# Optimization experiments

Measured on AMD Instinct MI355X. Metric: run time of the kernel, lower is better.

The kernel has to match this reference:

```python
import jax, jax.numpy as jnp
import numpy as np

K = 9          # top-k neighbors
GROUPS = 4     # GroupNorm groups
EPS_GN = 1e-5  # torch GroupNorm default eps


def group_norm(x, gamma, beta):
    # x: [B, C, H, W]; normalize over (C/GROUPS, H, W) per group
    B, C, H, W = x.shape
    xg = x.reshape(B, GROUPS, -1)
    mu = xg.mean(axis=-1, keepdims=True)
    var = xg.var(axis=-1, keepdims=True)
    xn = ((xg - mu) / jnp.sqrt(var + EPS_GN)).reshape(B, C, H, W)
    return xn * gamma[None, :, None, None] + beta[None, :, None, None]


def setup_inputs() -> dict:
    key = jax.random.key(0)
    ks = jax.random.split(key, 6)
    B, C, H, W = 32, 128, 45, 45
    std = 1.0 / np.sqrt(C)
    x = jax.random.normal(ks[0], (B, C, H, W), dtype=jnp.float32)
    w1 = jax.random.uniform(ks[1], (C, C), jnp.float32, -std, std)
    b1 = jax.random.uniform(ks[2], (C,), jnp.float32, -std, std)
    w2 = jax.random.uniform(ks[3], (C, C), jnp.float32, -std, std)
    b2 = jax.random.uniform(ks[4], (C,), jnp.float32, -std, std)
    gamma1 = jnp.ones((C,), jnp.float32)
    beta1 = jnp.zeros((C,), jnp.float32)
    gamma2 = jnp.ones((C,), jnp.float32)
    beta2 = jnp.zeros((C,), jnp.float32)
    return {"x": x, "w1": w1, "b1": b1, "w2": w2, "b2": b2,
            "gamma1": gamma1, "beta1": beta1, "gamma2": gamma2, "beta2": beta2}


def reference(x, w1, b1, w2, b2, gamma1, beta1, gamma2, beta2):
    B, C, H, W = x.shape
    N = H * W
    # build_knn: flatten, L2-normalize, cosine sim, top-k
    xf = x.reshape(B, C, N).transpose(0, 2, 1)                  # [B, N, C]
    nrm = jnp.linalg.norm(xf, axis=-1, keepdims=True)
    xn = xf / jnp.maximum(nrm, 1e-12)                           # F.normalize
    sim = jnp.einsum('bnc,bmc->bnm', xn, xn)                    # [B, N, N]
    val, idx = jax.lax.top_k(sim, K)                            # [B, N, K]
    # normalized edge weights (shared by both GCN layers)
    v = val / (val.sum(axis=-1, keepdims=True) + 1e-6)          # [B, N, K]

    def gcn_apply(feat, w, b):
        xt = feat @ w                                           # [B, N, C]
        neigh = jax.vmap(lambda t, i: t[i])(xt, idx)            # [B, N, K, C]
        return jnp.einsum('bnkc,bnk->bnc', neigh, v) + b

    out = gcn_apply(xn, w1, b1)
    out = jax.nn.silu(group_norm(out.transpose(0, 2, 1).reshape(B, C, H, W), gamma1, beta1))
    of = out.reshape(B, C, N).transpose(0, 2, 1)
    out = gcn_apply(of, w2, b2)
    out = jax.nn.silu(group_norm(out.transpose(0, 2, 1).reshape(B, C, H, W), gamma2, beta2))
    return out
```

## Files before the change

### kernel.cpp

```cpp
#include <hip/hip_runtime.h>
#include <hip/hip_bf16.h>

#define BN 32
#define CC 128
#define NN 2025
#define KK 9
#define NGROUP 4
#define CPG 32
#define GN_EPS 1e-5f
#define ROWS_TOTAL (BN * NN)

typedef _Float16 f16;
typedef __attribute__((ext_vector_type(8))) _Float16 f16x8;
typedef __attribute__((ext_vector_type(4))) _Float16 f16x4;
typedef __attribute__((ext_vector_type(4))) float f32x4;

#define S28 3.725290298461914e-09f
#define S40 9.094947017729282e-13f
#define S26 1.4901161193847656e-08f
#define S38 3.637978807091713e-12f
#define RH  6.103515625e-05f
#define RL  1.4901161193847656e-08f

#define T0F 0.17f
#define CAP 100

__global__ __launch_bounds__(256) void k_normalize(const float* __restrict__ x,
                                                   f16* __restrict__ xh, f16* __restrict__ xl) {
    __shared__ float tile[128][65];
    const int b  = blockIdx.y;
    const int n0 = blockIdx.x * 64;
    const int t  = threadIdx.x;
    const int w  = t >> 6;
    const int lane = t & 63;
    const int gn_ld = min(n0 + lane, NN - 1);

    for (int it = 0; it < 32; ++it) {
        int c = it * 4 + w;
        tile[c][lane] = x[((size_t)(b * CC + c)) * NN + gn_ld];
    }
    __syncthreads();

    for (int i = 0; i < 16; ++i) {
        int n  = w * 16 + i;
        int gn = n0 + n;
        if (gn < NN) {
            float v0 = tile[lane][n];
            float v1 = tile[lane + 64][n];
            float ss = v0 * v0 + v1 * v1;
#pragma unroll
            for (int off = 32; off > 0; off >>= 1) ss += __shfl_xor(ss, off);
            float s = 1.0f / fmaxf(sqrtf(ss), 1e-12f);
            v0 *= s; v1 *= s;
            float w0 = v0 * 16384.0f, w1 = v1 * 16384.0f;
            f16 h0 = (f16)w0, h1 = (f16)w1;
            f16 l0 = (f16)((w0 - (float)h0) * 4096.0f);
            f16 l1 = (f16)((w1 - (float)h1) * 4096.0f);
            size_t base = (size_t)(b * NN + gn) * CC;
            xh[base + lane] = h0;  xh[base + lane + 64] = h1;
            xl[base + lane] = l0;  xl[base + lane + 64] = l1;
        }
    }
}

__device__ __forceinline__ void ins9(float cand, int m, float* v, int* ix,
                                     float& mv, int& mi, int& mp) {
    bool take = (cand > mv) || ((cand == mv) && (m < mi));
    if (take) {
#pragma unroll
        for (int k = 0; k < 9; ++k) if (k == mp) { v[k] = cand; ix[k] = m; }
        float nv = v[0]; int ni = ix[0]; int np = 0;
#pragma unroll
        for (int k = 1; k < 9; ++k) {
            if (v[k] < nv || (v[k] == nv && ix[k] > ni)) { nv = v[k]; ni = ix[k]; np = k; }
        }
        mv = nv; mi = ni; mp = np;
    }
}

__global__ __launch_bounds__(256) void k_sim_topk(const f16* __restrict__ xh, const f16* __restrict__ xl,
                                                  float* __restrict__ vout, unsigned short* __restrict__ iout) {
    __shared__ f16x8          stg[2][32][16];
    __shared__ float          sv[32][CAP + 1];
    __shared__ unsigned short si[32][CAP + 2];
    __shared__ int   cnt[32];
    __shared__ int   nbad;
    __shared__ int   badrows[32];

    const int id   = blockIdx.x;
    const int b    = (id & 7) + 8 * (id >> 9);
    const int r0   = ((id >> 3) & 63) * 32;
    const int t    = threadIdx.x;
    const int w    = t >> 6;
    const int lane = t & 63;
    const int jr   = lane & 15;
    const int q    = lane >> 4;
    const int tw   = w & 1;
    const int mh   = w >> 1;

    if (t < 32) cnt[t] = 0;
    if (t == 0) nbad = 0;

    f16x8 bh[4], bl[4];
    {
        int rr = b * NN + min(r0 + tw * 16 + jr, NN - 1);
        const f16* pH = xh + (size_t)rr * CC;
        const f16* pL = xl + (size_t)rr * CC;
#pragma unroll
        for (int s = 0; s < 4; ++s) {
            bh[s] = *(const f16x8*)(pH + s * 32 + q * 8);
            bl[s] = *(const f16x8*)(pL + s * 32 + q * 8);
        }
    }

    const int fi_ = t & 15;
    const int ri_ = t >> 4;
    const int fx  = fi_ ^ (ri_ & 7);
    const int rbuf = tw * 16 + jr;

    f16x8 h0r, h1r, l0r, l1r;
    {
        size_t g0 = (size_t)(b * NN + min(ri_, NN - 1)) * CC + fi_ * 8;
        size_t g1 = (size_t)(b * NN + min(ri_ + 16, NN - 1)) * CC + fi_ * 8;
        h0r = *(const f16x8*)(xh + g0);  h1r = *(const f16x8*)(xh + g1);
        l0r = *(const f16x8*)(xl + g0);  l1r = *(const f16x8*)(xl + g1);
    }

    for (int chunk = 0; chunk < 64; ++chunk) {
        __syncthreads();
        stg[0][ri_][fx]      = h0r;
        stg[0][ri_ + 16][fx] = h1r;
        stg[1][ri_][fx]      = l0r;
        stg[1][ri_ + 16][fx] = l1r;
        __syncthreads();
        if (chunk < 63) {
            size_t g0 = (size_t)(b * NN + min((chunk + 1) * 32 + ri_, NN - 1)) * CC + fi_ * 8;
            size_t g1 = (size_t)(b * NN + min((chunk + 1) * 32 + ri_ + 16, NN - 1)) * CC + fi_ * 8;
            h0r = *(const f16x8*)(xh + g0);  h1r = *(const f16x8*)(xh + g1);
            l0r = *(const f16x8*)(xl + g0);  l1r = *(const f16x8*)(xl + g1);
        }
        __builtin_amdgcn_sched_barrier(0);

        const int mb   = chunk * 32 + mh * 16;
        const int arow = mh * 16 + jr;
        const int axr  = arow & 7;
        f32x4 hh = {0.f, 0.f, 0.f, 0.f}, ll = {0.f, 0.f, 0.f, 0.f};
#pragma unroll
        for (int s = 0; s < 4; ++s) {
            f16x8 ah = stg[0][arow][(s * 4 + q) ^ axr];
            f16x8 al = stg[1][arow][(s * 4 + q) ^ axr];
            hh = __builtin_amdgcn_mfma_f32_16x16x32_f16(ah, bh[s], hh, 0, 0, 0);
            ll = __builtin_amdgcn_mfma_f32_16x16x32_f16(ah, bl[s], ll, 0, 0, 0);
            ll = __builtin_amdgcn_mfma_f32_16x16x32_f16(al, bh[s], ll, 0, 0, 0);
        }
#pragma unroll
        for (int reg = 0; reg < 4; ++reg) {
            int m = mb + q * 4 + reg;
            float c0 = hh[reg] * S28 + ll[reg] * S40;
            if (m < NN && c0 > T0F) {
                int pos = atomicAdd(&cnt[rbuf], 1);
                if (pos < CAP) { sv[rbuf][pos] = c0; si[rbuf][pos] = (unsigned short)m; }
            }
        }
    }
    __syncthreads();

    if (t < 32) {
        int r = r0 + t;
        if (r < NN) {
            int c = cnt[t];
            if (c >= 9 && c <= CAP) {
                float fv[9]; int fi[9];
#pragma unroll
                for (int k = 0; k < 9; ++k) { fv[k] = -3.0e38f; fi[k] = 0x7fffffff; }
                float mv = -3.0e38f; int mi = 0x7fffffff; int mp = 0;
                for (int j = 0; j < c; ++j) ins9(sv[t][j], (int)si[t][j], fv, fi, mv, mi, mp);
                float s = 1e-6f;
#pragma unroll
                for (int k = 0; k < 9; ++k) s += fv[k];
                float inv = 1.0f / s;
                int base = (b * NN + r) * KK;
#pragma unroll
                for (int k = 0; k < 9; ++k) { vout[base + k] = fv[k] * inv; iout[base + k] = (unsigned short)fi[k]; }
            } else {
                int slot = atomicAdd(&nbad, 1);
                badrows[slot] = r;
            }
        }
    }
    __syncthreads();

    if (w == 0) {
        int nb = nbad;
        for (int ib = 0; ib < nb; ++ib) {
            int r = badrows[ib];
            const f16* rH = xh + ((size_t)b * NN + r) * CC;
            const f16* rL = xl + ((size_t)b * NN + r) * CC;
            float fv[9]; int fi[9];
#pragma unroll
            for (int k = 0; k < 9; ++k) { fv[k] = -3.0e38f; fi[k] = 0x7fffffff; }
            float mv = -3.0e38f; int mi = 0x7fffffff; int mp = 0;
            for (int m = lane; m < NN; m += 64) {
                const f16* mH = xh + ((size_t)b * NN + m) * CC;
                const f16* mL = xl + ((size_t)b * NN + m) * CC;
                float a1 = 0.f, a2 = 0.f;
                for (int c2 = 0; c2 < CC; ++c2) {
                    float hr = (float)rH[c2], hm = (float)mH[c2];
                    float lr = (float)rL[c2], lm = (float)mL[c2];
                    a1 += hr * hm;
                    a2 += hr * lm + lr * hm;
                }
                ins9(a1 * S28 + a2 * S40, m, fv, fi, mv, mi, mp);
            }
#pragma unroll
            for (int off = 1; off < 64; off <<= 1) {
                float pv[9]; int pi[9];
#pragma unroll
                for (int k = 0; k < 9; ++k) { pv[k] = __shfl_xor(fv[k], off); pi[k] = __shfl_xor(fi[k], off); }
#pragma unroll
                for (int k = 0; k < 9; ++k) ins9(pv[k], pi[k], fv, fi, mv, mi, mp);
            }
            if (lane == 0) {
                float s = 1e-6f;
#pragma unroll
                for (int k = 0; k < 9; ++k) s += fv[k];
                float inv = 1.0f / s;
                int base = (b * NN + r) * KK;
#pragma unroll
                for (int k = 0; k < 9; ++k) { vout[base + k] = fv[k] * inv; iout[base + k] = (unsigned short)fi[k]; }
            }
        }
    }
}

__global__ __launch_bounds__(256) void k_wsplit(const float* __restrict__ w1, const float* __restrict__ w2,
                                                f16* __restrict__ wth1, f16* __restrict__ wtl1,
                                                f16* __restrict__ wth2, f16* __restrict__ wtl2) {
    const float* w = blockIdx.x ? w2 : w1;
    f16* th = blockIdx.x ? wth2 : wth1;
    f16* tl = blockIdx.x ? wtl2 : wtl1;
    for (int e = threadIdx.x; e < CC * CC; e += 256) {
        int c = e >> 7, j = e & 127;
        float ws_ = w[e] * 16384.0f;
        f16 h = (f16)ws_;
        f16 l = (f16)((ws_ - (float)h) * 4096.0f);
        th[j * CC + c] = h;
        tl[j * CC + c] = l;
    }
}

__global__ __launch_bounds__(256) void k_gemm_mf(const f16* __restrict__ ah, const f16* __restrict__ al,
                                                 const f16* __restrict__ wth, const f16* __restrict__ wtl,
                                                 float sH, float sL, float* __restrict__ out) {
    const int t    = threadIdx.x;
    const int w    = t >> 6;
    const int lane = t & 63;
    const int jr   = lane & 15;
    const int q    = lane >> 4;
    const int row0 = blockIdx.x * 32;

    f16x8 wbh[2][4], wbl[2][4];
#pragma unroll
    for (int ct = 0; ct < 2; ++ct) {
        int j = w * 32 + ct * 16 + jr;
        const f16* pH = wth + (size_t)j * CC;
        const f16* pL = wtl + (size_t)j * CC;
#pragma unroll
        for (int s = 0; s < 4; ++s) {
            wbh[ct][s] = *(const f16x8*)(pH + s * 32 + q * 8);
            wbl[ct][s] = *(const f16x8*)(pL + s * 32 + q * 8);
        }
    }

#pragma unroll
    for (int rt = 0; rt < 2; ++rt) {
        int arow = row0 + rt * 16 + jr;
        const f16* pA  = ah + (size_t)arow * CC;
        const f16* pAl = al + (size_t)arow * CC;
        f16x8 af[4], alf[4];
#pragma unroll
        for (int s = 0; s < 4; ++s) {
            af[s]  = *(const f16x8*)(pA  + s * 32 + q * 8);
            alf[s] = *(const f16x8*)(pAl + s * 32 + q * 8);
        }
        f32x4 hh0 = {0.f,0.f,0.f,0.f}, ll0 = {0.f,0.f,0.f,0.f};
        f32x4 hh1 = {0.f,0.f,0.f,0.f}, ll1 = {0.f,0.f,0.f,0.f};
#pragma unroll
        for (int s = 0; s < 4; ++s) {
            hh0 = __builtin_amdgcn_mfma_f32_16x16x32_f16(af[s],  wbh[0][s], hh0, 0, 0, 0);
            ll0 = __builtin_amdgcn_mfma_f32_16x16x32_f16(af[s],  wbl[0][s], ll0, 0, 0, 0);
            ll0 = __builtin_amdgcn_mfma_f32_16x16x32_f16(alf[s], wbh[0][s], ll0, 0, 0, 0);
            hh1 = __builtin_amdgcn_mfma_f32_16x16x32_f16(af[s],  wbh[1][s], hh1, 0, 0, 0);
            ll1 = __builtin_amdgcn_mfma_f32_16x16x32_f16(af[s],  wbl[1][s], ll1, 0, 0, 0);
            ll1 = __builtin_amdgcn_mfma_f32_16x16x32_f16(alf[s], wbh[1][s], ll1, 0, 0, 0);
        }
#pragma unroll
        for (int reg = 0; reg < 4; ++reg) {
            int orow = row0 + rt * 16 + q * 4 + reg;
            size_t ob = (size_t)orow * CC + w * 32 + jr;
            out[ob]      = hh0[reg] * sH + ll0[reg] * sL;
            out[ob + 16] = hh1[reg] * sH + ll1[reg] * sL;
        }
    }
}

__global__ __launch_bounds__(256) void k_gather(const float* __restrict__ xt,
                                                const float* __restrict__ v,
                                                const unsigned short* __restrict__ idx,
                                                const float* __restrict__ bias,
                                                float* __restrict__ out) {
    int t = threadIdx.x;
    int g = blockIdx.x * 2 + (t >> 7);
    int c = t & 127;
    if (g >= ROWS_TOTAL) return;
    int b = g / NN;
    int nb = b * NN;
    float acc = bias[c];
    int base = g * KK;
#pragma unroll
    for (int k = 0; k < KK; ++k) {
        int   ii = (int)idx[base + k];
        float vv = v[base + k];
        acc += vv * xt[(size_t)(nb + ii) * CC + c];
    }
    out[(size_t)g * CC + c] = acc;
}

__global__ __launch_bounds__(256) void k_gnstats(const float* __restrict__ xin,
                                                 float* __restrict__ stats) {
    int bg = blockIdx.x; int b = bg >> 2; int gg = bg & 3;
    size_t base = (size_t)b * (NN * CC) + gg * CPG;
    float s1 = 0.f, s2 = 0.f;
    for (int i = threadIdx.x; i < NN * CPG; i += 256) {
        float x = xin[base + (size_t)(i >> 5) * CC + (i & 31)];
        s1 += x; s2 += x * x;
    }
#pragma unroll
    for (int off = 32; off > 0; off >>= 1) { s1 += __shfl_xor(s1, off); s2 += __shfl_xor(s2, off); }
    __shared__ float r1[4], r2[4];
    int w = threadIdx.x >> 6;
    if ((threadIdx.x & 63) == 0) { r1[w] = s1; r2[w] = s2; }
    __syncthreads();
    if (threadIdx.x == 0) {
        float a = r1[0] + r1[1] + r1[2] + r1[3];
        float qq = r2[0] + r2[1] + r2[2] + r2[3];
        const float inv = 1.0f / (float)(NN * CPG);
        float mean = a * inv;
        float var = qq * inv - mean * mean;
        stats[bg * 2]     = mean;
        stats[bg * 2 + 1] = rsqrtf(fmaxf(var, 0.f) + GN_EPS);
    }
}

__global__ __launch_bounds__(256) void k_gnsilu_split(const float* __restrict__ xin,
                                                      const float* __restrict__ stats,
                                                      const float* __restrict__ gamma,
                                                      const float* __restrict__ beta,
                                                      f16* __restrict__ vh, f16* __restrict__ vl) {
    size_t e4 = ((size_t)blockIdx.x * 256 + threadIdx.x) * 4;
    int c0 = (int)(e4 & 127);
    int b  = (int)(e4 / (NN * CC));
    int gg = c0 >> 5;
    float mean = stats[(b * 4 + gg) * 2];
    float rstd = stats[(b * 4 + gg) * 2 + 1];
    float4 x = *(const float4*)&xin[e4];
    float g0 = gamma[c0], g1 = gamma[c0 + 1], g2 = gamma[c0 + 2], g3 = gamma[c0 + 3];
    float p0 = beta[c0],  p1 = beta[c0 + 1],  p2 = beta[c0 + 2],  p3 = beta[c0 + 3];
    float y0 = (x.x - mean) * rstd * g0 + p0;
    float y1 = (x.y - mean) * rstd * g1 + p1;
    float y2 = (x.z - mean) * rstd * g2 + p2;
    float y3 = (x.w - mean) * rstd * g3 + p3;
    float r0 = y0 / (1.0f + expf(-y0));
    float r1 = y1 / (1.0f + expf(-y1));
    float r2 = y2 / (1.0f + expf(-y2));
    float r3 = y3 / (1.0f + expf(-y3));
    f16x4 hv, lv;
    float s0 = r0 * 4096.0f; hv[0] = (f16)s0; lv[0] = (f16)((s0 - (float)hv[0]) * 4096.0f);
    float s1 = r1 * 4096.0f; hv[1] = (f16)s1; lv[1] = (f16)((s1 - (float)hv[1]) * 4096.0f);
    float s2 = r2 * 4096.0f; hv[2] = (f16)s2; lv[2] = (f16)((s2 - (float)hv[2]) * 4096.0f);
    float s3 = r3 * 4096.0f; hv[3] = (f16)s3; lv[3] = (f16)((s3 - (float)hv[3]) * 4096.0f);
    *(f16x4*)&vh[e4] = hv;
    *(f16x4*)&vl[e4] = lv;
}

__global__ __launch_bounds__(256) void k_gnsilu_out(const float* __restrict__ xin,
                                                    const float* __restrict__ stats,
                                                    const float* __restrict__ gamma,
                                                    const float* __restrict__ beta,
                                                    float* __restrict__ out) {
    __shared__ float tile[32 * 65];
    int b = blockIdx.z, ct = blockIdx.y, nt = blockIdx.x;
    int c0 = ct * 32, n0 = nt * 64;
    int t = threadIdx.x;
    int cj = t & 31, ni0 = t >> 5;
    int gg = c0 >> 5;
    float mean = stats[(b * 4 + gg) * 2];
    float rstd = stats[(b * 4 + gg) * 2 + 1];
    float gm = gamma[c0 + cj];
    float bt = beta[c0 + cj];
#pragma unroll
    for (int i = 0; i < 8; ++i) {
        int n = n0 + ni0 + i * 8;
        if (n < NN) {
            float x = xin[((size_t)b * NN + n) * CC + c0 + cj];
            float y = (x - mean) * rstd * gm + bt;
            y = y / (1.0f + expf(-y));
            tile[cj * 65 + ni0 + i * 8] = y;
        }
    }
    __syncthreads();
    int nj = t & 63, ci0 = t >> 6;
#pragma unroll
    for (int i = 0; i < 8; ++i) {
        int c = ci0 + i * 4;
        int n = n0 + nj;
        if (n < NN) out[((size_t)b * CC + c0 + c) * NN + n] = tile[c * 65 + nj];
    }
}

extern "C" void kernel_launch(void* const* d_in, const int* in_sizes, int n_in,
                              void* d_out, int out_size, void* d_ws, size_t ws_size,
                              hipStream_t stream) {
    const float* x      = (const float*)d_in[0];
    const float* w1     = (const float*)d_in[1];
    const float* b1     = (const float*)d_in[2];
    const float* w2     = (const float*)d_in[3];
    const float* b2     = (const float*)d_in[4];
    const float* gamma1 = (const float*)d_in[5];
    const float* beta1  = (const float*)d_in[6];
    const float* gamma2 = (const float*)d_in[7];
    const float* beta2  = (const float*)d_in[8];
    float* out = (float*)d_out;

    const size_t BIG = (size_t)ROWS_TOTAL * CC;
    const size_t RK  = (size_t)ROWS_TOTAL * KK;
    float* ws   = (float*)d_ws;
    float* bufB = ws;
    f16*   xh   = (f16*)(ws + BIG);
    f16*   xl   = xh + BIG;
    float* bufA = ws + BIG;
    float* vbuf = ws + 2 * BIG;
    unsigned short* ibuf = (unsigned short*)(ws + 2 * BIG + RK);
    f16*   wth1 = (f16*)(ws + 2 * BIG + RK + RK / 2);
    f16*   wtl1 = wth1 + CC * CC;
    f16*   wth2 = wtl1 + CC * CC;
    f16*   wtl2 = wth2 + CC * CC;
    float* stats = ws + 2 * BIG + RK + RK / 2 + 2 * CC * CC;
    f16*   vh = (f16*)bufB;
    f16*   vl = vh + BIG;

    k_normalize<<<dim3(32, BN), 256, 0, stream>>>(x, xh, xl);
    k_wsplit<<<2, 256, 0, stream>>>(w1, w2, wth1, wtl1, wth2, wtl2);
    k_sim_topk<<<2048, 256, 0, stream>>>(xh, xl, vbuf, ibuf);

    k_gemm_mf<<<ROWS_TOTAL / 32, 256, 0, stream>>>(xh, xl, wth1, wtl1, S28, S40, bufB);
    k_gather<<<ROWS_TOTAL / 2, 256, 0, stream>>>(bufB, vbuf, ibuf, b1, bufA);
    k_gnstats<<<BN * NGROUP, 256, 0, stream>>>(bufA, stats);
    k_gnsilu_split<<<(int)(BIG / 1024), 256, 0, stream>>>(bufA, stats, gamma1, beta1, vh, vl);

    k_gemm_mf<<<ROWS_TOTAL / 32, 256, 0, stream>>>(vh, vl, wth2, wtl2, S26, S38, bufA);
    k_gather<<<ROWS_TOTAL / 2, 256, 0, stream>>>(bufA, vbuf, ibuf, b2, bufB);
    k_gnstats<<<BN * NGROUP, 256, 0, stream>>>(bufB, stats);
    k_gnsilu_out<<<dim3((NN + 63) / 64, NGROUP, BN), 256, 0, stream>>>(bufB, stats, gamma2, beta2, out);
}
```

Measured before the change: 671.6 us.

## Fuse GroupNorm+SiLU split into second GEMM and tile GEMM through swizzled LDS

Replaces the GEMM with a version that processes 128 rows per block in 32-row chunks. A-operand tiles are staged through XOR-swizzled shared memory, and the next chunk is prefetched into registers while the current one computes. Weight fragments are loaded once per block instead of once per 32 rows. The layer-1 GroupNorm+SiLU+fp16 split kernel is folded into the second GEMM's staging step, which removes a full write and read of the split activation buffers. The cost is more per-thread work (expf and splitting) inside the GEMM and fewer blocks.

```diff
diff --git a/kernel.cpp b/kernel.cpp
--- a/kernel.cpp
+++ b/kernel.cpp
@@ -12,15 +12,12 @@
 
 typedef _Float16 f16;
 typedef __attribute__((ext_vector_type(8))) _Float16 f16x8;
-typedef __attribute__((ext_vector_type(4))) _Float16 f16x4;
 typedef __attribute__((ext_vector_type(4))) float f32x4;
 
 #define S28 3.725290298461914e-09f
 #define S40 9.094947017729282e-13f
 #define S26 1.4901161193847656e-08f
 #define S38 3.637978807091713e-12f
-#define RH  6.103515625e-05f
-#define RL  1.4901161193847656e-08f
 
 #define T0F 0.17f
 #define CAP 100
@@ -249,15 +246,16 @@
     }
 }
 
-__global__ __launch_bounds__(256) void k_gemm_mf(const f16* __restrict__ ah, const f16* __restrict__ al,
-                                                 const f16* __restrict__ wth, const f16* __restrict__ wtl,
-                                                 float sH, float sL, float* __restrict__ out) {
+__global__ __launch_bounds__(256) void k_gemm_tile(const f16* __restrict__ ah, const f16* __restrict__ al,
+                                                   const f16* __restrict__ wth, const f16* __restrict__ wtl,
+                                                   float sH, float sL, float* __restrict__ out) {
+    __shared__ f16x8 stg[2][32][16];
     const int t    = threadIdx.x;
     const int w    = t >> 6;
     const int lane = t & 63;
     const int jr   = lane & 15;
     const int q    = lane >> 4;
-    const int row0 = blockIdx.x * 32;
+    const int row0 = blockIdx.x * 128;
 
     f16x8 wbh[2][4], wbl[2][4];
 #pragma unroll
@@ -272,34 +270,179 @@
         }
     }
 
-#pragma unroll
-    for (int rt = 0; rt < 2; ++rt) {
-        int arow = row0 + rt * 16 + jr;
-        const f16* pA  = ah + (size_t)arow * CC;
-        const f16* pAl = al + (size_t)arow * CC;
-        f16x8 af[4], alf[4];
+    const int fi_ = t & 15;
+    const int ri_ = t >> 4;
+    const int fx  = fi_ ^ (ri_ & 7);
+
+    f16x8 h0r, h1r, l0r, l1r;
+    {
+        size_t g0 = (size_t)min(row0 + ri_, ROWS_TOTAL - 1) * CC + fi_ * 8;
+        size_t g1 = (size_t)min(row0 + ri_ + 16, ROWS_TOTAL - 1) * CC + fi_ * 8;
+        h0r = *(const f16x8*)(ah + g0);  h1r = *(const f16x8*)(ah + g1);
+        l0r = *(const f16x8*)(al + g0);  l1r = *(const f16x8*)(al + g1);
+    }
+
+    for (int chunk = 0; chunk < 4; ++chunk) {
+        __syncthreads();
+        stg[0][ri_][fx]      = h0r;
+        stg[0][ri_ + 16][fx] = h1r;
+        stg[1][ri_][fx]      = l0r;
+        stg[1][ri_ + 16][fx] = l1r;
+        __syncthreads();
+        if (chunk < 3) {
+            size_t g0 = (size_t)min(row0 + (chunk + 1) * 32 + ri_, ROWS_TOTAL - 1) * CC + fi_ * 8;
+            size_t g1 = (size_t)min(row0 + (chunk + 1) * 32 + ri_ + 16, ROWS_TOTAL - 1) * CC + fi_ * 8;
+            h0r = *(const f16x8*)(ah + g0);  h1r = *(const f16x8*)(ah + g1);
+            l0r = *(const f16x8*)(al + g0);  l1r = *(const f16x8*)(al + g1);
+        }
+        __builtin_amdgcn_sched_barrier(0);
+
+#pragma unroll
+        for (int rt = 0; rt < 2; ++rt) {
+            const int arow = rt * 16 + jr;
+            const int axr  = arow & 7;
+            f16x8 af[4], alf[4];
+#pragma unroll
+            for (int s = 0; s < 4; ++s) {
+                af[s]  = stg[0][arow][(s * 4 + q) ^ axr];
+                alf[s] = stg[1][arow][(s * 4 + q) ^ axr];
+            }
+            f32x4 hh0 = {0.f,0.f,0.f,0.f}, ll0 = {0.f,0.f,0.f,0.f};
+            f32x4 hh1 = {0.f,0.f,0.f,0.f}, ll1 = {0.f,0.f,0.f,0.f};
+#pragma unroll
+            for (int s = 0; s < 4; ++s) {
+                hh0 = __builtin_amdgcn_mfma_f32_16x16x32_f16(af[s],  wbh[0][s], hh0, 0, 0, 0);
+                ll0 = __builtin_amdgcn_mfma_f32_16x16x32_f16(af[s],  wbl[0][s], ll0, 0, 0, 0);
+                ll0 = __builtin_amdgcn_mfma_f32_16x16x32_f16(alf[s], wbh[0][s], ll0, 0, 0, 0);
+                hh1 = __builtin_amdgcn_mfma_f32_16x16x32_f16(af[s],  wbh[1][s], hh1, 0, 0, 0);
+                ll1 = __builtin_amdgcn_mfma_f32_16x16x32_f16(af[s],  wbl[1][s], ll1, 0, 0, 0);
+                ll1 = __builtin_amdgcn_mfma_f32_16x16x32_f16(alf[s], wbh[1][s], ll1, 0, 0, 0);
+            }
+#pragma unroll
+            for (int reg = 0; reg < 4; ++reg) {
+                int orow = row0 + chunk * 32 + rt * 16 + q * 4 + reg;
+                if (orow < ROWS_TOTAL) {
+                    size_t ob = (size_t)orow * CC + w * 32 + jr;
+                    out[ob]      = hh0[reg] * sH + ll0[reg] * sL;
+                    out[ob + 16] = hh1[reg] * sH + ll1[reg] * sL;
+                }
+            }
+        }
+    }
+}
+
+__global__ __launch_bounds__(256) void k_gemm_tile_gn(const float* __restrict__ act,
+                                                      const float* __restrict__ stats,
+                                                      const float* __restrict__ gamma,
+                                                      const float* __restrict__ beta,
+                                                      const f16* __restrict__ wth, const f16* __restrict__ wtl,
+                                                      float sH, float sL, float* __restrict__ out) {
+    __shared__ f16x8 stg[2][32][16];
+    const int t    = threadIdx.x;
+    const int w    = t >> 6;
+    const int lane = t & 63;
+    const int jr   = lane & 15;
+    const int q    = lane >> 4;
+    const int row0 = blockIdx.x * 128;
+
+    f16x8 wbh[2][4], wbl[2][4];
+#pragma unroll
+    for (int ct = 0; ct < 2; ++ct) {
+        int j = w * 32 + ct * 16 + jr;
+        const f16* pH = wth + (size_t)j * CC;
+        const f16* pL = wtl + (size_t)j * CC;
 #pragma unroll
         for (int s = 0; s < 4; ++s) {
-            af[s]  = *(const f16x8*)(pA  + s * 32 + q * 8);
-            alf[s] = *(const f16x8*)(pAl + s * 32 + q * 8);
-        }
-        f32x4 hh0 = {0.f,0.f,0.f,0.f}, ll0 = {0.f,0.f,0.f,0.f};
-        f32x4 hh1 = {0.f,0.f,0.f,0.f}, ll1 = {0.f,0.f,0.f,0.f};
-#pragma unroll
-        for (int s = 0; s < 4; ++s) {
-            hh0 = __builtin_amdgcn_mfma_f32_16x16x32_f16(af[s],  wbh[0][s], hh0, 0, 0, 0);
-            ll0 = __builtin_amdgcn_mfma_f32_16x16x32_f16(af[s],  wbl[0][s], ll0, 0, 0, 0);
-            ll0 = __builtin_amdgcn_mfma_f32_16x16x32_f16(alf[s], wbh[0][s], ll0, 0, 0, 0);
-            hh1 = __builtin_amdgcn_mfma_f32_16x16x32_f16(af[s],  wbh[1][s], hh1, 0, 0, 0);
-            ll1 = __builtin_amdgcn_mfma_f32_16x16x32_f16(af[s],  wbl[1][s], ll1, 0, 0, 0);
-            ll1 = __builtin_amdgcn_mfma_f32_16x16x32_f16(alf[s], wbh[1][s], ll1, 0, 0, 0);
-        }
-#pragma unroll
-        for (int reg = 0; reg < 4; ++reg) {
-            int orow = row0 + rt * 16 + q * 4 + reg;
-            size_t ob = (size_t)orow * CC + w * 32 + jr;
-            out[ob]      = hh0[reg] * sH + ll0[reg] * sL;
-            out[ob + 16] = hh1[reg] * sH + ll1[reg] * sL;
+            wbh[ct][s] = *(const f16x8*)(pH + s * 32 + q * 8);
+            wbl[ct][s] = *(const f16x8*)(pL + s * 32 + q * 8);
+        }
+    }
+
+    const int fi_ = t & 15;
+    const int ri_ = t >> 4;
+    const int fx  = fi_ ^ (ri_ & 7);
+    const int gg  = fi_ >> 2;
+
+    float gma[8], bta[8];
+#pragma unroll
+    for (int e = 0; e < 8; ++e) { gma[e] = gamma[fi_ * 8 + e]; bta[e] = beta[fi_ * 8 + e]; }
+
+    float4 pa0, pa1, pb0, pb1;
+    int ra = min(row0 + ri_, ROWS_TOTAL - 1);
+    int rb = min(row0 + ri_ + 16, ROWS_TOTAL - 1);
+    {
+        const float* p0 = act + (size_t)ra * CC + fi_ * 8;
+        const float* p1 = act + (size_t)rb * CC + fi_ * 8;
+        pa0 = *(const float4*)p0;  pa1 = *(const float4*)(p0 + 4);
+        pb0 = *(const float4*)p1;  pb1 = *(const float4*)(p1 + 4);
+    }
+
+    for (int chunk = 0; chunk < 4; ++chunk) {
+        __syncthreads();
+        {
+            float va[8] = {pa0.x, pa0.y, pa0.z, pa0.w, pa1.x, pa1.y, pa1.z, pa1.w};
+            float vb[8] = {pb0.x, pb0.y, pb0.z, pb0.w, pb1.x, pb1.y, pb1.z, pb1.w};
+            int ba = ra / NN, bb = rb / NN;
+            float ma = stats[(ba * 4 + gg) * 2], rsa = stats[(ba * 4 + gg) * 2 + 1];
+            float mb = stats[(bb * 4 + gg) * 2], rsb = stats[(bb * 4 + gg) * 2 + 1];
+            f16x8 hva, lva, hvb, lvb;
+#pragma unroll
+            for (int e = 0; e < 8; ++e) {
+                float ya = (va[e] - ma) * rsa * gma[e] + bta[e];
+                float ra_ = ya / (1.0f + expf(-ya));
+                float sa = ra_ * 4096.0f;
+                f16 h = (f16)sa; hva[e] = h; lva[e] = (f16)((sa - (float)h) * 4096.0f);
+                float yb = (vb[e] - mb) * rsb * gma[e] + bta[e];
+                float rb_ = yb / (1.0f + expf(-yb));
+                float sb = rb_ * 4096.0f;
+                f16 h2 = (f16)sb; hvb[e] = h2; lvb[e] = (f16)((sb - (float)h2) * 4096.0f);
+            }
+            stg[0][ri_][fx]      = hva;
+            stg[0][ri_ + 16][fx] = hvb;
+            stg[1][ri_][fx]      = lva;
+            stg[1][ri_ + 16][fx] = lvb;
+        }
+        __syncthreads();
+        if (chunk < 3) {
+            ra = min(row0 + (chunk + 1) * 32 + ri_, ROWS_TOTAL - 1);
+            rb = min(row0 + (chunk + 1) * 32 + ri_ + 16, ROWS_TOTAL - 1);
+            const float* p0 = act + (size_t)ra * CC + fi_ * 8;
+            const float* p1 = act + (size_t)rb * CC + fi_ * 8;
+            pa0 = *(const float4*)p0;  pa1 = *(const float4*)(p0 + 4);
+            pb0 = *(const float4*)p1;  pb1 = *(const float4*)(p1 + 4);
+        }
+        __builtin_amdgcn_sched_barrier(0);
+
+#pragma unroll
+        for (int rt = 0; rt < 2; ++rt) {
+            const int arow = rt * 16 + jr;
+            const int axr  = arow & 7;
+            f16x8 af[4], alf[4];
+#pragma unroll
+            for (int s = 0; s < 4; ++s) {
+                af[s]  = stg[0][arow][(s * 4 + q) ^ axr];
+                alf[s] = stg[1][arow][(s * 4 + q) ^ axr];
+            }
+            f32x4 hh0 = {0.f,0.f,0.f,0.f}, ll0 = {0.f,0.f,0.f,0.f};
+            f32x4 hh1 = {0.f,0.f,0.f,0.f}, ll1 = {0.f,0.f,0.f,0.f};
+#pragma unroll
+            for (int s = 0; s < 4; ++s) {
+                hh0 = __builtin_amdgcn_mfma_f32_16x16x32_f16(af[s],  wbh[0][s], hh0, 0, 0, 0);
+                ll0 = __builtin_amdgcn_mfma_f32_16x16x32_f16(af[s],  wbl[0][s], ll0, 0, 0, 0);
+                ll0 = __builtin_amdgcn_mfma_f32_16x16x32_f16(alf[s], wbh[0][s], ll0, 0, 0, 0);
+                hh1 = __builtin_amdgcn_mfma_f32_16x16x32_f16(af[s],  wbh[1][s], hh1, 0, 0, 0);
+                ll1 = __builtin_amdgcn_mfma_f32_16x16x32_f16(af[s],  wbl[1][s], ll1, 0, 0, 0);
+                ll1 = __builtin_amdgcn_mfma_f32_16x16x32_f16(alf[s], wbh[1][s], ll1, 0, 0, 0);
+            }
+#pragma unroll
+            for (int reg = 0; reg < 4; ++reg) {
+                int orow = row0 + chunk * 32 + rt * 16 + q * 4 + reg;
+                if (orow < ROWS_TOTAL) {
+                    size_t ob = (size_t)orow * CC + w * 32 + jr;
+                    out[ob]      = hh0[reg] * sH + ll0[reg] * sL;
+                    out[ob + 16] = hh1[reg] * sH + ll1[reg] * sL;
+                }
+            }
         }
     }
 }
@@ -350,37 +493,6 @@
         stats[bg * 2]     = mean;
         stats[bg * 2 + 1] = rsqrtf(fmaxf(var, 0.f) + GN_EPS);
     }
-}
-
-__global__ __launch_bounds__(256) void k_gnsilu_split(const float* __restrict__ xin,
-                                                      const float* __restrict__ stats,
-                                                      const float* __restrict__ gamma,
-                                                      const float* __restrict__ beta,
-                                                      f16* __restrict__ vh, f16* __restrict__ vl) {
-    size_t e4 = ((size_t)blockIdx.x * 256 + threadIdx.x) * 4;
-    int c0 = (int)(e4 & 127);
-    int b  = (int)(e4 / (NN * CC));
-    int gg = c0 >> 5;
-    float mean = stats[(b * 4 + gg) * 2];
-    float rstd = stats[(b * 4 + gg) * 2 + 1];
-    float4 x = *(const float4*)&xin[e4];
-    float g0 = gamma[c0], g1 = gamma[c0 + 1], g2 = gamma[c0 + 2], g3 = gamma[c0 + 3];
-    float p0 = beta[c0],  p1 = beta[c0 + 1],  p2 = beta[c0 + 2],  p3 = beta[c0 + 3];
-    float y0 = (x.x - mean) * rstd * g0 + p0;
-    float y1 = (x.y - mean) * rstd * g1 + p1;
-    float y2 = (x.z - mean) * rstd * g2 + p2;
-    float y3 = (x.w - mean) * rstd * g3 + p3;
-    float r0 = y0 / (1.0f + expf(-y0));
-    float r1 = y1 / (1.0f + expf(-y1));
-    float r2 = y2 / (1.0f + expf(-y2));
-    float r3 = y3 / (1.0f + expf(-y3));
-    f16x4 hv, lv;
-    float s0 = r0 * 4096.0f; hv[0] = (f16)s0; lv[0] = (f16)((s0 - (float)hv[0]) * 4096.0f);
-    float s1 = r1 * 4096.0f; hv[1] = (f16)s1; lv[1] = (f16)((s1 - (float)hv[1]) * 4096.0f);
-    float s2 = r2 * 4096.0f; hv[2] = (f16)s2; lv[2] = (f16)((s2 - (float)hv[2]) * 4096.0f);
-    float s3 = r3 * 4096.0f; hv[3] = (f16)s3; lv[3] = (f16)((s3 - (float)hv[3]) * 4096.0f);
-    *(f16x4*)&vh[e4] = hv;
-    *(f16x4*)&vl[e4] = lv;
 }
 
 __global__ __launch_bounds__(256) void k_gnsilu_out(const float* __restrict__ xin,
@@ -446,20 +558,19 @@
     f16*   wth2 = wtl1 + CC * CC;
     f16*   wtl2 = wth2 + CC * CC;
     float* stats = ws + 2 * BIG + RK + RK / 2 + 2 * CC * CC;
-    f16*   vh = (f16*)bufB;
-    f16*   vl = vh + BIG;
+
+    const int GB = (ROWS_TOTAL + 127) / 128;
 
     k_normalize<<<dim3(32, BN), 256, 0, stream>>>(x, xh, xl);
     k_wsplit<<<2, 256, 0, stream>>>(w1, w2, wth1, wtl1, wth2, wtl2);
     k_sim_topk<<<2048, 256, 0, stream>>>(xh, xl, vbuf, ibuf);
 
-    k_gemm_mf<<<ROWS_TOTAL / 32, 256, 0, stream>>>(xh, xl, wth1, wtl1, S28, S40, bufB);
+    k_gemm_tile<<<GB, 256, 0, stream>>>(xh, xl, wth1, wtl1, S28, S40, bufB);
     k_gather<<<ROWS_TOTAL / 2, 256, 0, stream>>>(bufB, vbuf, ibuf, b1, bufA);
     k_gnstats<<<BN * NGROUP, 256, 0, stream>>>(bufA, stats);
-    k_gnsilu_split<<<(int)(BIG / 1024), 256, 0, stream>>>(bufA, stats, gamma1, beta1, vh, vl);
-
-    k_gemm_mf<<<ROWS_TOTAL / 32, 256, 0, stream>>>(vh, vl, wth2, wtl2, S26, S38, bufA);
-    k_gather<<<ROWS_TOTAL / 2, 256, 0, stream>>>(bufA, vbuf, ibuf, b2, bufB);
-    k_gnstats<<<BN * NGROUP, 256, 0, stream>>>(bufB, stats);
-    k_gnsilu_out<<<dim3((NN + 63) / 64, NGROUP, BN), 256, 0, stream>>>(bufB, stats, gamma2, beta2, out);
-}
+
+    k_gemm_tile_gn<<<GB, 256, 0, stream>>>(bufA, stats, gamma1, beta1, wth2, wtl2, S26, S38, bufB);
+    k_gather<<<ROWS_TOTAL / 2, 256, 0, stream>>>(bufB, vbuf, ibuf, b2, bufA);
+    k_gnstats<<<BN * NGROUP, 256, 0, stream>>>(bufA, stats);
+    k_gnsilu_out<<<dim3((NN + 63) / 64, NGROUP, BN), 256, 0, stream>>>(bufA, stats, gamma2, beta2, out);
+}
```

After: 629.8 us. -6.2%, faster.
